# Optimization experiments

Measured on AMD Instinct MI355X. Metric: run time of the kernel, lower is better.

## Reference

```python
import jax, jax.numpy as jnp
import numpy as np

N_NODES = 100000
N_EDGES = 1600000
D_IN = 64
D_HID = 64


def setup_inputs() -> dict:
    key = jax.random.key(0)
    k_x, k_e, k_wl, k_wr, k_b = jax.random.split(key, 5)
    x = jax.random.normal(k_x, (N_NODES, D_IN), dtype=jnp.float32)
    edge_index = jax.random.randint(k_e, (2, N_EDGES), 0, N_NODES, dtype=jnp.int64)
    # SAGEConv params: lin_l (applied to aggregated neighbors, has bias),
    # lin_r (applied to root/self, no bias). Stored as [in, out] for x @ W.
    scale = 1.0 / np.sqrt(D_IN)
    W_l = jax.random.uniform(k_wl, (D_IN, D_HID), jnp.float32, -scale, scale)
    W_r = jax.random.uniform(k_wr, (D_IN, D_HID), jnp.float32, -scale, scale)
    b = jax.random.uniform(k_b, (D_HID,), jnp.float32, -scale, scale)
    return {"x": x, "edge_index": edge_index, "W_l": W_l, "W_r": W_r, "b": b}


def reference(x, edge_index, W_l, W_r, b):
    # GraphSAGE 1-layer: mean-aggregate neighbor feats, linear, add root term, ReLU.
    src = edge_index[0]  # message sources (neighbors j)
    dst = edge_index[1]  # message targets (nodes i)
    n = x.shape[0]
    msg = x[src]  # [E, D_IN] irregular gather
    s = jax.ops.segment_sum(msg, dst, num_segments=n)  # [N, D_IN]
    cnt = jax.ops.segment_sum(jnp.ones((src.shape[0],), x.dtype), dst, num_segments=n)
    agg = s / jnp.maximum(cnt, 1.0)[:, None]  # mean aggregation
    out = agg @ W_l + x @ W_r + b  # SAGEConv: lin_l(agg) + lin_r(x)
    return jax.nn.relu(out)
```

## Files before the change

### kernel.cpp

```cpp
#include <hip/hip_runtime.h>
#include <hip/hip_bf16.h>

#define D 64
#define CHUNK 4096
#define NBKT_SHIFT 7
#define NSUB 8
#define SUBCAP 720
#define CAPB (NSUB * SUBCAP)
#define LCAP 48

typedef __attribute__((ext_vector_type(8))) short short8;
typedef __attribute__((ext_vector_type(4))) float f32x4;

__device__ __forceinline__ unsigned short f2b(float f) {
    unsigned u = __float_as_uint(f);
    return (unsigned short)((u + 0x7FFFu + ((u >> 16) & 1u)) >> 16);
}
__device__ __forceinline__ float b2f(unsigned short s) {
    return __uint_as_float((unsigned)s << 16);
}

__global__ __launch_bounds__(256, 4) void k_combo(
        const float* __restrict__ x, const int* __restrict__ src,
        const int* __restrict__ dst, const float* __restrict__ Wl,
        const float* __restrict__ Wr, const float* __restrict__ b,
        int* __restrict__ cursor, int* __restrict__ pairs,
        unsigned short* __restrict__ ylb, float* __restrict__ out,
        int nE, int nN, int nB, int nA, int total) {
    __shared__ __align__(16) char smem[27648];

    const int bid = blockIdx.x;
    const int t = threadIdx.x;

    const long long lo = ((long long)bid * nA) / total;
    const long long hi = ((long long)(bid + 1) * nA) / total;

    if (hi > lo) {
        int* hA = (int*)smem;
        int* bL = hA + 800;
        const int chunk = (int)lo;
        const int e0 = chunk * CHUNK;
        const int cnt = min(CHUNK, nE - e0);
        const int sub = chunk & (NSUB - 1);

        int rd[16], rs[16], rr[16];
#pragma unroll
        for (int j = 0; j < 16; ++j) {
            int i = t + j * 256;
            rd[j] = (i < cnt) ? dst[e0 + i] : -1;
        }
#pragma unroll
        for (int j = 0; j < 16; ++j) {
            int i = t + j * 256;
            rs[j] = (i < cnt) ? src[e0 + i] : 0;
        }

        for (int i = t; i < nB; i += 256) hA[i] = 0;
        __syncthreads();
#pragma unroll
        for (int j = 0; j < 16; ++j)
            rr[j] = (rd[j] >= 0) ? atomicAdd(&hA[rd[j] >> NBKT_SHIFT], 1) : 0;
        __syncthreads();
        const int start = (chunk * 401) % nB;
        for (int i = t; i < nB; i += 256) {
            int bk = i + start; if (bk >= nB) bk -= nB;
            int c = hA[bk];
            bL[bk] = (c > 0) ? atomicAdd(&cursor[bk * NSUB + sub], c) : 0;
        }
        __syncthreads();
#pragma unroll
        for (int j = 0; j < 16; ++j) {
            int d = rd[j];
            if (d < 0) continue;
            int bk = d >> NBKT_SHIFT;
            int p = bL[bk] + rr[j];
            if (p < SUBCAP)
                pairs[(size_t)bk * CAPB + sub * SUBCAP + p] = ((d & 127) << 17) | rs[j];
        }
        return;
    }

    const int g = bid - (int)lo;
    const int tile = g * 64;
    const int l = t & 63, w = t >> 6;

    short* sWl  = (short*)smem;
    short* sWrh = sWl + 4608;
    short* sWrl = sWrh + 4608;
    {
        const int n0 = (t & 15) * 4;
        const int kp = t >> 4;
#pragma unroll
        for (int i = 0; i < 2; ++i) {
            const int k = 2 * (kp + 16 * i);
            float4 l0 = *(const float4*)&Wl[k * 64 + n0];
            float4 l1 = *(const float4*)&Wl[(k + 1) * 64 + n0];
            float4 r0 = *(const float4*)&Wr[k * 64 + n0];
            float4 r1 = *(const float4*)&Wr[(k + 1) * 64 + n0];
            float fl0[4] = {l0.x, l0.y, l0.z, l0.w};
            float fl1[4] = {l1.x, l1.y, l1.z, l1.w};
            float fr0[4] = {r0.x, r0.y, r0.z, r0.w};
            float fr1[4] = {r1.x, r1.y, r1.z, r1.w};
#pragma unroll
            for (int c = 0; c < 4; ++c) {
                const int n = n0 + c;
                const int addr = n * 72 + ((((k >> 3) + 2 * n) & 7) << 3) + (k & 7);
                *(unsigned*)&sWl[addr] =
                    (unsigned)f2b(fl0[c]) | ((unsigned)f2b(fl1[c]) << 16);
                unsigned short h0 = f2b(fr0[c]), h1 = f2b(fr1[c]);
                *(unsigned*)&sWrh[addr] = (unsigned)h0 | ((unsigned)h1 << 16);
                unsigned short g0 = f2b(fr0[c] - b2f(h0));
                unsigned short g1 = f2b(fr1[c] - b2f(h1));
                *(unsigned*)&sWrl[addr] = (unsigned)g0 | ((unsigned)g1 << 16);
            }
        }
    }

    const int qrow = w * 16 + (l & 15);
    const int gg = tile + qrow;
    const int g4 = l >> 4;
    float4 z4 = {0.f, 0.f, 0.f, 0.f};
    float4 xa = z4, xb = z4, xc = z4, xd = z4;
    if (gg < nN) {
        const float4* xr = (const float4*)(x + (size_t)gg * D);
        xa = xr[2 * g4];     xb = xr[2 * g4 + 1];
        xc = xr[2 * g4 + 8]; xd = xr[2 * g4 + 9];
    }
    short8 ah0, al0, ah1, al1;
    {
        float f0[8] = {xa.x, xa.y, xa.z, xa.w, xb.x, xb.y, xb.z, xb.w};
        float f1[8] = {xc.x, xc.y, xc.z, xc.w, xd.x, xd.y, xd.z, xd.w};
#pragma unroll
        for (int i = 0; i < 8; ++i) {
            unsigned short h = f2b(f0[i]);
            ah0[i] = (short)h; al0[i] = (short)f2b(f0[i] - b2f(h));
            unsigned short h2 = f2b(f1[i]);
            ah1[i] = (short)h2; al1[i] = (short)f2b(f1[i] - b2f(h2));
        }
    }
    __syncthreads();

    f32x4 accl[4] = {}, accr[4] = {};
#pragma unroll
    for (int kh = 0; kh < 2; ++kh) {
        short8 AH = kh ? ah1 : ah0;
        short8 AL = kh ? al1 : al0;
        const int K8 = kh * 4 + g4;
#pragma unroll
        for (int ns = 0; ns < 4; ++ns) {
            const int col = ns * 16 + (l & 15);
            const int coff = col * 72 + (((K8 + 2 * col) & 7) << 3);
            short8 bl  = *(short8*)&sWl[coff];
            short8 brh = *(short8*)&sWrh[coff];
            short8 brl = *(short8*)&sWrl[coff];
            accl[ns] = __builtin_amdgcn_mfma_f32_16x16x32_bf16(AH, bl,  accl[ns], 0, 0, 0);
            accl[ns] = __builtin_amdgcn_mfma_f32_16x16x32_bf16(AL, bl,  accl[ns], 0, 0, 0);
            accr[ns] = __builtin_amdgcn_mfma_f32_16x16x32_bf16(AH, brh, accr[ns], 0, 0, 0);
            accr[ns] = __builtin_amdgcn_mfma_f32_16x16x32_bf16(AH, brl, accr[ns], 0, 0, 0);
            accr[ns] = __builtin_amdgcn_mfma_f32_16x16x32_bf16(AL, brh, accr[ns], 0, 0, 0);
        }
    }

    __syncthreads();
    float* sOut = (float*)smem;
    unsigned short* sYl = (unsigned short*)(smem + 17408);
#pragma unroll
    for (int ns = 0; ns < 4; ++ns) {
        const int col = ns * 16 + (l & 15);
        const float bv = b[col];
#pragma unroll
        for (int r = 0; r < 4; ++r) {
            const int rl = w * 16 + (l >> 4) * 4 + r;
            sOut[rl * 68 + col] = accr[ns][r] + bv;
            sYl[rl * 72 + col] = f2b(accl[ns][r]);
        }
    }
    __syncthreads();
    {
        const int row = t >> 2, cq = t & 3;
        const int gn = tile + row;
        if (gn < nN) {
            float4* po = (float4*)&out[(size_t)gn * D + cq * 16];
#pragma unroll
            for (int i = 0; i < 4; ++i)
                po[i] = *(const float4*)&sOut[row * 68 + cq * 16 + i * 4];
        }
    }
    if (t < 128) {
        const int row = t >> 1, hf = t & 1;
        const int gn = tile + row;
        if (gn < nN) {
            const uint4* sv = (const uint4*)&sYl[row * 72 + hf * 32];
            uint4* pv = (uint4*)&ylb[(size_t)gn * D + hf * 32];
            pv[0] = sv[0]; pv[1] = sv[1]; pv[2] = sv[2]; pv[3] = sv[3];
        }
    }
}

#define ACC8(p) {                                        \
    a0 += __uint_as_float((p).x << 16);                  \
    a1 += __uint_as_float((p).x & 0xffff0000u);          \
    a2 += __uint_as_float((p).y << 16);                  \
    a3 += __uint_as_float((p).y & 0xffff0000u);          \
    a4 += __uint_as_float((p).z << 16);                  \
    a5 += __uint_as_float((p).z & 0xffff0000u);          \
    a6 += __uint_as_float((p).w << 16);                  \
    a7 += __uint_as_float((p).w & 0xffff0000u); }

__global__ __launch_bounds__(256) void k_gather2(
        const uint4* __restrict__ ylbv, const int* __restrict__ cursor,
        const int* __restrict__ pairs, float* __restrict__ out, int nN) {
    __shared__ int lists[32 * LCAP];
    __shared__ int c32[32];
    __shared__ int sC[8];

    const int nwg = gridDim.x;
    const int q = nwg >> 3, r = nwg & 7;
    const int xcd = blockIdx.x & 7, ix = blockIdx.x >> 3;
    const int g = (xcd < r ? xcd * (q + 1) : r * (q + 1) + (xcd - r) * q) + ix;

    const int t = threadIdx.x;
    const int bkt = g >> 2;
    const int qd = g & 3;

    if (t < 32) c32[t] = 0;
    if (t < 8) sC[t] = min(cursor[bkt * NSUB + t], SUBCAP);
    __syncthreads();

    const size_t pbase = (size_t)bkt * CAPB;
    {
        int sub = 0, pos = t;
#pragma unroll 4
        for (int k = 0; k < 23; ++k) {
            if (sub < NSUB && pos < sC[sub]) {
                int v = pairs[pbase + sub * SUBCAP + pos];
                int dl = v >> 17;
                if ((dl >> 5) == qd) {
                    int rk = atomicAdd(&c32[dl & 31], 1);
                    if (rk < LCAP) lists[(dl & 31) * LCAP + rk] = v & 0x1FFFF;
                }
            }
            pos += 256;
            if (pos >= SUBCAP) { pos -= SUBCAP; ++sub; }
        }
    }
    __syncthreads();

    const int nl = t >> 3, l = t & 7;
    const int node = bkt * 128 + qd * 32 + nl;
    if (node >= nN) return;
    const int deg = c32[nl];
    const int n = min(deg, LCAP);

    float4* po = (float4*)&out[(size_t)node * D + l * 8];
    float4 r0 = po[0], r1 = po[1];

    float a0 = 0.f, a1 = 0.f, a2 = 0.f, a3 = 0.f;
    float a4 = 0.f, a5 = 0.f, a6 = 0.f, a7 = 0.f;

    int k = 0;
    for (; k + 8 <= n; k += 8) {
        int4 iv0 = *(const int4*)&lists[nl * LCAP + k];
        int4 iv1 = *(const int4*)&lists[nl * LCAP + k + 4];
        uint4 p0 = ylbv[(size_t)iv0.x * 8 + l];
        uint4 p1 = ylbv[(size_t)iv0.y * 8 + l];
        uint4 p2 = ylbv[(size_t)iv0.z * 8 + l];
        uint4 p3 = ylbv[(size_t)iv0.w * 8 + l];
        uint4 p4 = ylbv[(size_t)iv1.x * 8 + l];
        uint4 p5 = ylbv[(size_t)iv1.y * 8 + l];
        uint4 p6 = ylbv[(size_t)iv1.z * 8 + l];
        uint4 p7 = ylbv[(size_t)iv1.w * 8 + l];
        ACC8(p0); ACC8(p1); ACC8(p2); ACC8(p3);
        ACC8(p4); ACC8(p5); ACC8(p6); ACC8(p7);
    }
    for (; k + 4 <= n; k += 4) {
        int4 iv = *(const int4*)&lists[nl * LCAP + k];
        uint4 p0 = ylbv[(size_t)iv.x * 8 + l];
        uint4 p1 = ylbv[(size_t)iv.y * 8 + l];
        uint4 p2 = ylbv[(size_t)iv.z * 8 + l];
        uint4 p3 = ylbv[(size_t)iv.w * 8 + l];
        ACC8(p0); ACC8(p1); ACC8(p2); ACC8(p3);
    }
    for (; k < n; ++k) {
        uint4 p = ylbv[(size_t)lists[nl * LCAP + k] * 8 + l];
        ACC8(p);
    }

    const float inv = 1.f / fmaxf((float)deg, 1.f);
    r0.x = fmaxf(a0 * inv + r0.x, 0.f);
    r0.y = fmaxf(a1 * inv + r0.y, 0.f);
    r0.z = fmaxf(a2 * inv + r0.z, 0.f);
    r0.w = fmaxf(a3 * inv + r0.w, 0.f);
    r1.x = fmaxf(a4 * inv + r1.x, 0.f);
    r1.y = fmaxf(a5 * inv + r1.y, 0.f);
    r1.z = fmaxf(a6 * inv + r1.z, 0.f);
    r1.w = fmaxf(a7 * inv + r1.w, 0.f);
    po[0] = r0; po[1] = r1;
}

extern "C" void kernel_launch(void* const* d_in, const int* in_sizes, int n_in,
                              void* d_out, int out_size, void* d_ws, size_t ws_size,
                              hipStream_t stream) {
    const float* x  = (const float*)d_in[0];
    const int*   ei = (const int*)d_in[1];
    const float* Wl = (const float*)d_in[2];
    const float* Wr = (const float*)d_in[3];
    const float* b  = (const float*)d_in[4];
    float*       out = (float*)d_out;

    const int nN = in_sizes[0] / D;
    const int nE = in_sizes[1] / 2;
    const int* src = ei;
    const int* dst = ei + nE;

    const int nB = (nN + 127) >> NBKT_SHIFT;

    int* cursor = (int*)d_ws;
    int* pairs  = cursor + (size_t)nB * NSUB;
    size_t off = (size_t)nB * NSUB + (size_t)nB * CAPB;
    off = (off + 63) & ~(size_t)63;
    unsigned short* ylb = (unsigned short*)((int*)d_ws + off);

    hipMemsetAsync(cursor, 0, (size_t)nB * NSUB * sizeof(int), stream);

    const int nA    = (nE + CHUNK - 1) / CHUNK;
    const int nPre  = (nN + 63) / 64;
    const int total = nA + nPre;

    k_combo<<<total, 256, 0, stream>>>(x, src, dst, Wl, Wr, b,
                                       cursor, pairs, ylb, out, nE, nN, nB, nA, total);
    k_gather2<<<(nN + 31) / 32, 256, 0, stream>>>((const uint4*)ylb, cursor,
                                                  pairs, out, nN);
}
```

Measured before the change: 158.4 us.

## Merge scatter, precompute and gather into one persistent kernel with grid barrier

Replaces the two-kernel launch with a single persistent kernel of 1024 blocks. The blocks pull work items from per-XCD atomic counters, first for scatter and precompute, then for gather, and a global spin barrier on a done counter separates the two phases. The intent is to remove the second launch and its tail gap and to balance load dynamically. In exchange it adds atomic work-fetch overhead and a spin-wait barrier. The barrier also relies on every block being co-resident, so it can deadlock if occupancy does not allow that.

```diff
diff --git a/kernel.cpp b/kernel.cpp
--- a/kernel.cpp
+++ b/kernel.cpp
@@ -8,6 +8,7 @@
 #define SUBCAP 720
 #define CAPB (NSUB * SUBCAP)
 #define LCAP 48
+#define GRID 1024
 
 typedef __attribute__((ext_vector_type(8))) short short8;
 typedef __attribute__((ext_vector_type(4))) float f32x4;
@@ -20,67 +21,59 @@
     return __uint_as_float((unsigned)s << 16);
 }
 
-__global__ __launch_bounds__(256, 4) void k_combo(
-        const float* __restrict__ x, const int* __restrict__ src,
-        const int* __restrict__ dst, const float* __restrict__ Wl,
-        const float* __restrict__ Wr, const float* __restrict__ b,
-        int* __restrict__ cursor, int* __restrict__ pairs,
-        unsigned short* __restrict__ ylb, float* __restrict__ out,
-        int nE, int nN, int nB, int nA, int total) {
-    __shared__ __align__(16) char smem[27648];
-
-    const int bid = blockIdx.x;
+__device__ __forceinline__ void scatter_item(
+        char* smem, int chunk, const int* __restrict__ src,
+        const int* __restrict__ dst, int* __restrict__ cursor,
+        int* __restrict__ pairs, int nE, int nB) {
+    int* hA = (int*)smem;
+    int* bL = hA + 800;
     const int t = threadIdx.x;
-
-    const long long lo = ((long long)bid * nA) / total;
-    const long long hi = ((long long)(bid + 1) * nA) / total;
-
-    if (hi > lo) {
-        int* hA = (int*)smem;
-        int* bL = hA + 800;
-        const int chunk = (int)lo;
-        const int e0 = chunk * CHUNK;
-        const int cnt = min(CHUNK, nE - e0);
-        const int sub = chunk & (NSUB - 1);
-
-        int rd[16], rs[16], rr[16];
-#pragma unroll
-        for (int j = 0; j < 16; ++j) {
-            int i = t + j * 256;
-            rd[j] = (i < cnt) ? dst[e0 + i] : -1;
-        }
-#pragma unroll
-        for (int j = 0; j < 16; ++j) {
-            int i = t + j * 256;
-            rs[j] = (i < cnt) ? src[e0 + i] : 0;
-        }
-
-        for (int i = t; i < nB; i += 256) hA[i] = 0;
-        __syncthreads();
-#pragma unroll
-        for (int j = 0; j < 16; ++j)
-            rr[j] = (rd[j] >= 0) ? atomicAdd(&hA[rd[j] >> NBKT_SHIFT], 1) : 0;
-        __syncthreads();
-        const int start = (chunk * 401) % nB;
-        for (int i = t; i < nB; i += 256) {
-            int bk = i + start; if (bk >= nB) bk -= nB;
-            int c = hA[bk];
-            bL[bk] = (c > 0) ? atomicAdd(&cursor[bk * NSUB + sub], c) : 0;
-        }
-        __syncthreads();
-#pragma unroll
-        for (int j = 0; j < 16; ++j) {
-            int d = rd[j];
-            if (d < 0) continue;
-            int bk = d >> NBKT_SHIFT;
-            int p = bL[bk] + rr[j];
-            if (p < SUBCAP)
-                pairs[(size_t)bk * CAPB + sub * SUBCAP + p] = ((d & 127) << 17) | rs[j];
-        }
-        return;
-    }
-
-    const int g = bid - (int)lo;
+    const int e0 = chunk * CHUNK;
+    const int cnt = min(CHUNK, nE - e0);
+    const int sub = chunk & (NSUB - 1);
+
+    int rd[16], rs[16], rr[16];
+#pragma unroll
+    for (int j = 0; j < 16; ++j) {
+        int i = t + j * 256;
+        rd[j] = (i < cnt) ? dst[e0 + i] : -1;
+    }
+#pragma unroll
+    for (int j = 0; j < 16; ++j) {
+        int i = t + j * 256;
+        rs[j] = (i < cnt) ? src[e0 + i] : 0;
+    }
+
+    for (int i = t; i < nB; i += 256) hA[i] = 0;
+    __syncthreads();
+#pragma unroll
+    for (int j = 0; j < 16; ++j)
+        rr[j] = (rd[j] >= 0) ? atomicAdd(&hA[rd[j] >> NBKT_SHIFT], 1) : 0;
+    __syncthreads();
+    const int start = (chunk * 401) % nB;
+    for (int i = t; i < nB; i += 256) {
+        int bk = i + start; if (bk >= nB) bk -= nB;
+        int c = hA[bk];
+        bL[bk] = (c > 0) ? atomicAdd(&cursor[bk * NSUB + sub], c) : 0;
+    }
+    __syncthreads();
+#pragma unroll
+    for (int j = 0; j < 16; ++j) {
+        int d = rd[j];
+        if (d < 0) continue;
+        int bk = d >> NBKT_SHIFT;
+        int p = bL[bk] + rr[j];
+        if (p < SUBCAP)
+            pairs[(size_t)bk * CAPB + sub * SUBCAP + p] = ((d & 127) << 17) | rs[j];
+    }
+}
+
+__device__ __forceinline__ void pre_item(
+        char* smem, int g, const float* __restrict__ x,
+        const float* __restrict__ Wl, const float* __restrict__ Wr,
+        const float* __restrict__ b, unsigned short* __restrict__ ylb,
+        float* __restrict__ out, int nN) {
+    const int t = threadIdx.x;
     const int tile = g * 64;
     const int l = t & 63, w = t >> 6;
 
@@ -207,21 +200,16 @@
     a6 += __uint_as_float((p).w << 16);                  \
     a7 += __uint_as_float((p).w & 0xffff0000u); }
 
-__global__ __launch_bounds__(256) void k_gather2(
-        const uint4* __restrict__ ylbv, const int* __restrict__ cursor,
-        const int* __restrict__ pairs, float* __restrict__ out, int nN) {
-    __shared__ int lists[32 * LCAP];
-    __shared__ int c32[32];
-    __shared__ int sC[8];
-
-    const int nwg = gridDim.x;
-    const int q = nwg >> 3, r = nwg & 7;
-    const int xcd = blockIdx.x & 7, ix = blockIdx.x >> 3;
-    const int g = (xcd < r ? xcd * (q + 1) : r * (q + 1) + (xcd - r) * q) + ix;
-
+__device__ __forceinline__ void gather_item(
+        char* smem, int it, const uint4* __restrict__ ylbv,
+        const int* __restrict__ cursor, const int* __restrict__ pairs,
+        float* __restrict__ out, int nN) {
+    int* lists = (int*)smem;
+    int* c32   = lists + 32 * LCAP;
+    int* sC    = c32 + 32;
     const int t = threadIdx.x;
-    const int bkt = g >> 2;
-    const int qd = g & 3;
+    const int bkt = it >> 2;
+    const int qd = it & 3;
 
     if (t < 32) c32[t] = 0;
     if (t < 8) sC[t] = min(cursor[bkt * NSUB + t], SUBCAP);
@@ -248,54 +236,105 @@
 
     const int nl = t >> 3, l = t & 7;
     const int node = bkt * 128 + qd * 32 + nl;
-    if (node >= nN) return;
-    const int deg = c32[nl];
-    const int n = min(deg, LCAP);
-
-    float4* po = (float4*)&out[(size_t)node * D + l * 8];
-    float4 r0 = po[0], r1 = po[1];
-
-    float a0 = 0.f, a1 = 0.f, a2 = 0.f, a3 = 0.f;
-    float a4 = 0.f, a5 = 0.f, a6 = 0.f, a7 = 0.f;
-
-    int k = 0;
-    for (; k + 8 <= n; k += 8) {
-        int4 iv0 = *(const int4*)&lists[nl * LCAP + k];
-        int4 iv1 = *(const int4*)&lists[nl * LCAP + k + 4];
-        uint4 p0 = ylbv[(size_t)iv0.x * 8 + l];
-        uint4 p1 = ylbv[(size_t)iv0.y * 8 + l];
-        uint4 p2 = ylbv[(size_t)iv0.z * 8 + l];
-        uint4 p3 = ylbv[(size_t)iv0.w * 8 + l];
-        uint4 p4 = ylbv[(size_t)iv1.x * 8 + l];
-        uint4 p5 = ylbv[(size_t)iv1.y * 8 + l];
-        uint4 p6 = ylbv[(size_t)iv1.z * 8 + l];
-        uint4 p7 = ylbv[(size_t)iv1.w * 8 + l];
-        ACC8(p0); ACC8(p1); ACC8(p2); ACC8(p3);
-        ACC8(p4); ACC8(p5); ACC8(p6); ACC8(p7);
-    }
-    for (; k + 4 <= n; k += 4) {
-        int4 iv = *(const int4*)&lists[nl * LCAP + k];
-        uint4 p0 = ylbv[(size_t)iv.x * 8 + l];
-        uint4 p1 = ylbv[(size_t)iv.y * 8 + l];
-        uint4 p2 = ylbv[(size_t)iv.z * 8 + l];
-        uint4 p3 = ylbv[(size_t)iv.w * 8 + l];
-        ACC8(p0); ACC8(p1); ACC8(p2); ACC8(p3);
-    }
-    for (; k < n; ++k) {
-        uint4 p = ylbv[(size_t)lists[nl * LCAP + k] * 8 + l];
-        ACC8(p);
-    }
-
-    const float inv = 1.f / fmaxf((float)deg, 1.f);
-    r0.x = fmaxf(a0 * inv + r0.x, 0.f);
-    r0.y = fmaxf(a1 * inv + r0.y, 0.f);
-    r0.z = fmaxf(a2 * inv + r0.z, 0.f);
-    r0.w = fmaxf(a3 * inv + r0.w, 0.f);
-    r1.x = fmaxf(a4 * inv + r1.x, 0.f);
-    r1.y = fmaxf(a5 * inv + r1.y, 0.f);
-    r1.z = fmaxf(a6 * inv + r1.z, 0.f);
-    r1.w = fmaxf(a7 * inv + r1.w, 0.f);
-    po[0] = r0; po[1] = r1;
+    if (node < nN) {
+        const int deg = c32[nl];
+        const int n = min(deg, LCAP);
+
+        float4* po = (float4*)&out[(size_t)node * D + l * 8];
+        float4 r0 = po[0], r1 = po[1];
+
+        float a0 = 0.f, a1 = 0.f, a2 = 0.f, a3 = 0.f;
+        float a4 = 0.f, a5 = 0.f, a6 = 0.f, a7 = 0.f;
+
+        int k = 0;
+        for (; k + 8 <= n; k += 8) {
+            int4 iv0 = *(const int4*)&lists[nl * LCAP + k];
+            int4 iv1 = *(const int4*)&lists[nl * LCAP + k + 4];
+            uint4 p0 = ylbv[(size_t)iv0.x * 8 + l];
+            uint4 p1 = ylbv[(size_t)iv0.y * 8 + l];
+            uint4 p2 = ylbv[(size_t)iv0.z * 8 + l];
+            uint4 p3 = ylbv[(size_t)iv0.w * 8 + l];
+            uint4 p4 = ylbv[(size_t)iv1.x * 8 + l];
+            uint4 p5 = ylbv[(size_t)iv1.y * 8 + l];
+            uint4 p6 = ylbv[(size_t)iv1.z * 8 + l];
+            uint4 p7 = ylbv[(size_t)iv1.w * 8 + l];
+            ACC8(p0); ACC8(p1); ACC8(p2); ACC8(p3);
+            ACC8(p4); ACC8(p5); ACC8(p6); ACC8(p7);
+        }
+        for (; k + 4 <= n; k += 4) {
+            int4 iv = *(const int4*)&lists[nl * LCAP + k];
+            uint4 p0 = ylbv[(size_t)iv.x * 8 + l];
+            uint4 p1 = ylbv[(size_t)iv.y * 8 + l];
+            uint4 p2 = ylbv[(size_t)iv.z * 8 + l];
+            uint4 p3 = ylbv[(size_t)iv.w * 8 + l];
+            ACC8(p0); ACC8(p1); ACC8(p2); ACC8(p3);
+        }
+        for (; k < n; ++k) {
+            uint4 p = ylbv[(size_t)lists[nl * LCAP + k] * 8 + l];
+            ACC8(p);
+        }
+
+        const float inv = 1.f / fmaxf((float)deg, 1.f);
+        r0.x = fmaxf(a0 * inv + r0.x, 0.f);
+        r0.y = fmaxf(a1 * inv + r0.y, 0.f);
+        r0.z = fmaxf(a2 * inv + r0.z, 0.f);
+        r0.w = fmaxf(a3 * inv + r0.w, 0.f);
+        r1.x = fmaxf(a4 * inv + r1.x, 0.f);
+        r1.y = fmaxf(a5 * inv + r1.y, 0.f);
+        r1.z = fmaxf(a6 * inv + r1.z, 0.f);
+        r1.w = fmaxf(a7 * inv + r1.w, 0.f);
+        po[0] = r0; po[1] = r1;
+    }
+}
+
+__global__ __launch_bounds__(256, 4) void k_all(
+        const float* __restrict__ x, const int* __restrict__ src,
+        const int* __restrict__ dst, const float* __restrict__ Wl,
+        const float* __restrict__ Wr, const float* __restrict__ b,
+        int* __restrict__ ctr, int* __restrict__ cursor,
+        int* __restrict__ pairs, unsigned short* __restrict__ ylb,
+        float* __restrict__ out, int nE, int nN, int nB,
+        int nA, int nW1, int nW2) {
+    __shared__ __align__(16) char smem[27648];
+    __shared__ int sIt;
+    const int t = threadIdx.x;
+
+    int myDone = 0;
+    const int c0 = blockIdx.x & 7;
+    for (int d = 0; d < 8; ++d) {
+        const int c = (c0 + d) & 7;
+        for (;;) {
+            if (t == 0) sIt = c + 8 * atomicAdd(&ctr[c * 16], 1);
+            __syncthreads();
+            const int it = sIt;
+            __syncthreads();
+            if (it >= nW1) break;
+            if (it < nA) scatter_item(smem, it, src, dst, cursor, pairs, nE, nB);
+            else         pre_item(smem, it - nA, x, Wl, Wr, b, ylb, out, nN);
+            ++myDone;
+        }
+    }
+    __threadfence();
+    if (t == 0 && myDone) atomicAdd(&ctr[128], myDone);
+    if (t == 0) {
+        while (__hip_atomic_load(&ctr[128], __ATOMIC_ACQUIRE,
+                                 __HIP_MEMORY_SCOPE_AGENT) < nW1)
+            __builtin_amdgcn_s_sleep(8);
+    }
+    __syncthreads();
+    __threadfence();
+
+    for (int d = 0; d < 8; ++d) {
+        const int c = (c0 + d) & 7;
+        for (;;) {
+            if (t == 0) sIt = c + 8 * atomicAdd(&ctr[144 + c * 16], 1);
+            __syncthreads();
+            const int it = sIt;
+            __syncthreads();
+            if (it >= nW2) break;
+            gather_item(smem, it, (const uint4*)ylb, cursor, pairs, out, nN);
+        }
+    }
 }
 
 extern "C" void kernel_launch(void* const* d_in, const int* in_sizes, int n_in,
@@ -315,20 +354,20 @@
 
     const int nB = (nN + 127) >> NBKT_SHIFT;
 
-    int* cursor = (int*)d_ws;
+    int* ctr    = (int*)d_ws;
+    int* cursor = ctr + 1024;
     int* pairs  = cursor + (size_t)nB * NSUB;
-    size_t off = (size_t)nB * NSUB + (size_t)nB * CAPB;
+    size_t off = 1024 + (size_t)nB * NSUB + (size_t)nB * CAPB;
     off = (off + 63) & ~(size_t)63;
     unsigned short* ylb = (unsigned short*)((int*)d_ws + off);
 
-    hipMemsetAsync(cursor, 0, (size_t)nB * NSUB * sizeof(int), stream);
-
-    const int nA    = (nE + CHUNK - 1) / CHUNK;
-    const int nPre  = (nN + 63) / 64;
-    const int total = nA + nPre;
-
-    k_combo<<<total, 256, 0, stream>>>(x, src, dst, Wl, Wr, b,
-                                       cursor, pairs, ylb, out, nE, nN, nB, nA, total);
-    k_gather2<<<(nN + 31) / 32, 256, 0, stream>>>((const uint4*)ylb, cursor,
-                                                  pairs, out, nN);
-}
+    hipMemsetAsync(ctr, 0, (1024 + (size_t)nB * NSUB) * sizeof(int), stream);
+
+    const int nA  = (nE + CHUNK - 1) / CHUNK;
+    const int nW1 = nA + (nN + 63) / 64;
+    const int nW2 = nB * 4;
+
+    k_all<<<GRID, 256, 0, stream>>>(x, src, dst, Wl, Wr, b,
+                                    ctr, cursor, pairs, ylb, out,
+                                    nE, nN, nB, nA, nW1, nW2);
+}
```

After: 459.6 us. 2.9x slower.
